# Kernel optimization log

Hardware: AMD Instinct MI355X
Metric: run time of the kernel (lower is better)

The kernel has to match this reference:

```python
import jax, jax.numpy as jnp
import numpy as np

W_DIM, T_DIM = 300, 100
IN = W_DIM + T_DIM        # 400, also LSTM hidden size
H = IN                    # hiddenSize
BI = 2 * H                # 800, biLSTM output per step
MLP_IN = 2 * BI           # 1600
VOCAB, NTAGS = 50000, 50
SEQ = 320


def _lstm_dir(xs, w_ih, w_hh, b_ih, b_hh, h0, c0, reverse):
    # xs: [T, d_in]; PyTorch gate order i, f, g, o
    if reverse:
        xs = xs[::-1]
    def step(carry, x):
        h, c = carry
        g = x @ w_ih.T + h @ w_hh.T + b_ih + b_hh
        i, f, gc, o = jnp.split(g, 4)
        i, f, o = jax.nn.sigmoid(i), jax.nn.sigmoid(f), jax.nn.sigmoid(o)
        c = f * c + i * jnp.tanh(gc)
        h = o * jnp.tanh(c)
        return (h, c), h
    _, ys = jax.lax.scan(step, (h0, c0), xs)
    return ys[::-1] if reverse else ys


def _bilstm(x, params, h0, c0):
    # x: [T, IN]; h0/c0: [4, H] ordered (l0 fwd, l0 bwd, l1 fwd, l1 bwd)
    out = x
    for layer in range(2):
        p_f = params[layer][0]
        p_b = params[layer][1]
        yf = _lstm_dir(out, *p_f, h0[2 * layer],     c0[2 * layer],     False)
        yb = _lstm_dir(out, *p_b, h0[2 * layer + 1], c0[2 * layer + 1], True)
        out = jnp.concatenate([yf, yb], axis=-1)  # [T, 2H]
    return out


def setup_inputs() -> dict:
    key = jax.random.key(0)
    ks = iter(jax.random.split(key, 32))
    inp = {}
    inp['words'] = jax.random.randint(next(ks), (SEQ,), 0, VOCAB)
    inp['tags'] = jax.random.randint(next(ks), (SEQ,), 0, NTAGS)
    inp['arcs'] = jax.random.randint(next(ks), (SEQ + 1,), 0, SEQ + 1)
    inp['word_emb'] = jax.random.normal(next(ks), (VOCAB, W_DIM), jnp.float32) * 0.1
    inp['tag_emb'] = jax.random.normal(next(ks), (NTAGS, T_DIM), jnp.float32) * 0.1
    inp['h0'] = jax.random.normal(next(ks), (4, H), jnp.float32)
    inp['c0'] = jax.random.normal(next(ks), (4, H), jnp.float32)
    s = 1.0 / np.sqrt(H)
    for layer, d_in in ((0, IN), (1, BI)):
        for suf in ('', 'r'):
            inp[f'w_ih_l{layer}{suf}'] = jax.random.uniform(next(ks), (4 * H, d_in), jnp.float32, -s, s)
            inp[f'w_hh_l{layer}{suf}'] = jax.random.uniform(next(ks), (4 * H, H), jnp.float32, -s, s)
            inp[f'b_ih_l{layer}{suf}'] = jax.random.uniform(next(ks), (4 * H,), jnp.float32, -s, s)
            inp[f'b_hh_l{layer}{suf}'] = jax.random.uniform(next(ks), (4 * H,), jnp.float32, -s, s)
    inp['mlp_w1'] = jax.random.normal(next(ks), (MLP_IN, MLP_IN), jnp.float32) * 0.02
    inp['mlp_b1'] = jnp.zeros((MLP_IN,), jnp.float32)
    inp['mlp_w2'] = jax.random.normal(next(ks), (1, MLP_IN), jnp.float32) * 0.02
    inp['mlp_b2'] = jnp.zeros((1,), jnp.float32)
    return inp


def reference(words, tags, arcs, word_emb, tag_emb, h0, c0,
              w_ih_l0, w_hh_l0, b_ih_l0, b_hh_l0,
              w_ih_l0r, w_hh_l0r, b_ih_l0r, b_hh_l0r,
              w_ih_l1, w_hh_l1, b_ih_l1, b_hh_l1,
              w_ih_l1r, w_hh_l1r, b_ih_l1r, b_hh_l1r,
              mlp_w1, mlp_b1, mlp_w2, mlp_b2):
    n = words.shape[0]
    x = jnp.concatenate([word_emb[words], tag_emb[tags]], axis=1)  # [n, IN]
    params = (((w_ih_l0, w_hh_l0, b_ih_l0, b_hh_l0), (w_ih_l0r, w_hh_l0r, b_ih_l0r, b_hh_l0r)),
              ((w_ih_l1, w_hh_l1, b_ih_l1, b_hh_l1), (w_ih_l1r, w_hh_l1r, b_ih_l1r, b_hh_l1r)))
    hv = _bilstm(x, params, h0, c0)  # [n, BI]
    # pairwise MLP: concat(h_head, h_dep) @ W1.T == h_head @ W1a.T + h_dep @ W1b.T
    w1a, w1b = mlp_w1[:, :BI], mlp_w1[:, BI:]
    a = hv @ w1a.T  # [n, MLP_IN], head part
    b = hv @ w1b.T  # [n, MLP_IN], dep part
    hid = jax.nn.relu(a[:, None, :] + b[None, :, :] + mlp_b1)  # [n, n, MLP_IN]
    scores = jnp.einsum('ndk,ok->nd', hid, mlp_w2)[..., 0] if mlp_w2.shape[0] != 1 else (hid @ mlp_w2[0] + mlp_b2[0])  # [n, n]
    offdiag = 1.0 - jnp.eye(n, dtype=scores.dtype)
    score_tensor = jnp.zeros((n + 1, n + 1), scores.dtype)
    score_tensor = score_tensor.at[0, 0].set(1.0)
    score_tensor = score_tensor.at[1:, 1:].set(scores * offdiag)
    return score_tensor
```

## Files before the change

kernel.cpp:

```cpp
#include <hip/hip_runtime.h>
#include <hip/hip_bf16.h>
#include <hip/hip_fp16.h>

#define SEQ   320
#define GATES 1600
#define NCOL  3200
#define GDW   16
#define RPW   25

typedef _Float16 half2v __attribute__((ext_vector_type(2)));
typedef _Float16 f16x8  __attribute__((ext_vector_type(8)));
typedef float    f32x4  __attribute__((ext_vector_type(4)));
union H2U { unsigned u; half2v h; __half2 hh; };

__global__ __launch_bounds__(256) void prep_kernel(
    const int* __restrict__ words, const int* __restrict__ tags,
    const float* __restrict__ wemb, const float* __restrict__ temb,
    _Float16* __restrict__ Ah0,
    const float* __restrict__ bihl0,  const float* __restrict__ bhhl0,
    const float* __restrict__ bihl0r, const float* __restrict__ bhhl0r,
    const float* __restrict__ bihl1,  const float* __restrict__ bhhl1,
    const float* __restrict__ bihl1r, const float* __restrict__ bhhl1r,
    const float* __restrict__ mlpb1,
    float* __restrict__ bL0, float* __restrict__ bL1, float* __restrict__ bAB,
    const float* __restrict__ wih0, const float* __restrict__ wih0r,
    _Float16* __restrict__ BhA)
{
    const int b = blockIdx.x, t = threadIdx.x;
    if (b < 520) {
        int i = b * 256 + t;
        if (i >= SEQ * 416) return;
        int tt = i / 416, c = i % 416;
        float v = 0.f;
        if (c < 300)      v = wemb[(size_t)words[tt] * 300 + c];
        else if (c < 400) v = temb[(size_t)tags[tt] * 100 + (c - 300)];
        Ah0[i] = (_Float16)v;
    } else if (b < 533) {
        int g = (b - 520) * 256 + t;
        if (g >= NCOL) return;
        if (g < GATES) {
            bL0[g] = bihl0[g] + bhhl0[g];
            bL1[g] = bihl1[g] + bhhl1[g];
            bAB[g] = mlpb1[g];
        } else {
            int q = g - GATES;
            bL0[g] = bihl0r[q] + bhhl0r[q];
            bL1[g] = bihl1r[q] + bhhl1r[q];
            bAB[g] = 0.f;
        }
    } else {
        int i = (b - 533) * 256 + t;
        if (i >= NCOL * 416) return;
        int n = i / 416, k = i % 416;
        float v = 0.f;
        if (k < 400)
            v = (n < GATES) ? wih0[(size_t)n * 400 + k]
                            : wih0r[(size_t)(n - GATES) * 400 + k];
        BhA[i] = (_Float16)v;
    }
}

__global__ __launch_bounds__(256) void cvt2_kernel(
    const float* __restrict__ wih1, const float* __restrict__ wih1r,
    _Float16* __restrict__ BhB,
    const float* __restrict__ mlpw1, _Float16* __restrict__ BhA)
{
    const int b = blockIdx.x, t = threadIdx.x;
    if (b < 10000) {
        int i = b * 256 + t;
        if (i >= NCOL * 800) return;
        int n = i / 800, k = i % 800;
        BhB[i] = (_Float16)((n < GATES) ? wih1[(size_t)n * 800 + k]
                                        : wih1r[(size_t)(n - GATES) * 800 + k]);
    } else {
        int i = (b - 10000) * 256 + t;
        if (i >= NCOL * 800) return;
        int n = i / 800, k = i % 800;
        BhA[i] = (_Float16)((n < GATES) ? mlpw1[(size_t)n * 1600 + k]
                                        : mlpw1[(size_t)(n - GATES) * 1600 + 800 + k]);
    }
}

__global__ __launch_bounds__(256) void gemm_f16(
    const _Float16* __restrict__ A, int Kp,
    const _Float16* __restrict__ B,
    const float* __restrict__ bias, float* __restrict__ C)
{
    const int tid  = threadIdx.x;
    const int w    = tid >> 6, lane = tid & 63;
    const int quad = lane >> 4, l16 = lane & 15;
    const int mb   = blockIdx.y * 32 + (w & 1) * 16;
    const int n0   = blockIdx.x * 64 + (w >> 1) * 32;
    const _Float16* Arow = A + (size_t)(mb + l16) * Kp + quad * 8;
    const _Float16* B0r  = B + (size_t)(n0 + l16) * Kp + quad * 8;
    const _Float16* B1r  = B0r + (size_t)16 * Kp;
    f32x4 acc0 = {0.f, 0.f, 0.f, 0.f}, acc1 = {0.f, 0.f, 0.f, 0.f};
#pragma unroll 4
    for (int k0 = 0; k0 < Kp; k0 += 32) {
        f16x8 a  = *(const f16x8*)(Arow + k0);
        f16x8 b0 = *(const f16x8*)(B0r + k0);
        f16x8 b1 = *(const f16x8*)(B1r + k0);
        acc0 = __builtin_amdgcn_mfma_f32_16x16x32_f16(a, b0, acc0, 0, 0, 0);
        acc1 = __builtin_amdgcn_mfma_f32_16x16x32_f16(a, b1, acc1, 0, 0, 0);
    }
    const int mr = mb + quad * 4;
    float bn0 = bias[n0 + l16], bn1 = bias[n0 + 16 + l16];
#pragma unroll
    for (int r = 0; r < 4; ++r) {
        C[(size_t)(mr + r) * NCOL + n0 + l16]      = acc0[r] + bn0;
        C[(size_t)(mr + r) * NCOL + n0 + 16 + l16] = acc1[r] + bn1;
    }
}

__global__ __launch_bounds__(1024, 4) void lstm_layer(
    const float* __restrict__ gates,
    const float* __restrict__ whh_f, const float* __restrict__ whh_b,
    const float* __restrict__ h0f, const float* __restrict__ h0b,
    const float* __restrict__ c0f, const float* __restrict__ c0b,
    unsigned* __restrict__ ex,
    _Float16* __restrict__ ah)
{
    __shared__ unsigned h_pk[200];
    __shared__ float part[16][28];
    unsigned short* hs = (unsigned short*)h_pk;
    const int tid = threadIdx.x;
    const int dir = blockIdx.x >> 4;
    const int wg  = blockIdx.x & 15;
    const int j0  = wg * RPW;
    const float* whh = dir ? whh_b : whh_f;
    const float* h0d = dir ? h0b : h0f;
    const float* c0d = dir ? c0b : c0f;

    const int w    = tid >> 6;
    const int lane = tid & 63;
    const int g    = w & 3;
    const int kq   = w >> 2;
    const int half = lane & 1;
    const int r    = lane >> 1;
    const int jrow = j0 + (r < RPW ? r : RPW - 1);

    unsigned wr[26];
    {
        const float2* wp = (const float2*)(whh + (size_t)(g * 400 + jrow) * 400 +
                                           kq * 100 + 48 * half);
#pragma unroll
        for (int i = 0; i < 26; ++i) {
            H2U cv; float2 f = wp[i];
            cv.hh = __floats2half2_rn(f.x, f.y);
            wr[i] = (half == 0 && i >= 24) ? 0u : cv.u;
        }
    }

    const int pp = tid / 13;
    const int pd = tid - pp * 13;
    float c_prev = (tid < RPW) ? c0d[j0 + tid] : 0.f;

    for (int s = 0; s < 320; ++s) {
        const int row = dir ? (319 - s) : s;

        float gv0 = 0.f, gv1 = 0.f, gv2 = 0.f, gv3 = 0.f;
        if (tid < RPW) {
            const float* gx = gates + (size_t)row * NCOL + dir * GATES + j0 + tid;
            gv0 = gx[0]; gv1 = gx[400]; gv2 = gx[800]; gv3 = gx[1200];
        }

        if (s == 0) {
            if (tid < 100) {
                float4 f = ((const float4*)h0d)[tid];
                H2U a, b;
                a.hh = __floats2half2_rn(f.x, f.y);
                b.hh = __floats2half2_rn(f.z, f.w);
                ((uint2*)h_pk)[tid] = make_uint2(a.u, b.u);
            }
        } else if (tid < 208 && pp != wg) {
            const int rp = dir ? (row + 1) : (row - 1);
            const unsigned* src = ex + (((size_t)dir * GDW + pp) * SEQ + rp) * 16 + pd;
            unsigned v;
            for (;;) {
                v = __hip_atomic_load(src, __ATOMIC_RELAXED, __HIP_MEMORY_SCOPE_AGENT);
                if ((v & 0xFFFFu) != 0xFFFFu &&
                    (pd == 12 || (v >> 16) != 0xFFFFu)) break;
            }
            const int hb = pp * RPW + pd * 2;
            hs[hb] = (unsigned short)(v & 0xFFFFu);
            if (pd < 12) hs[hb + 1] = (unsigned short)(v >> 16);
        }
        __syncthreads();

        {
            const uint2* hp2 = (const uint2*)h_pk + kq * 25 + 12 * half;
            float acc = 0.f;
#pragma unroll
            for (int i = 0; i < 13; ++i) {
                uint2 hv2 = hp2[i];
                H2U w0, w1, x0, x1;
                w0.u = wr[2 * i]; w1.u = wr[2 * i + 1];
                x0.u = hv2.x;     x1.u = hv2.y;
                acc = __builtin_amdgcn_fdot2(w0.h, x0.h, acc, false);
                acc = __builtin_amdgcn_fdot2(w1.h, x1.h, acc, false);
            }
            acc += __shfl_xor(acc, 1, 64);
            if (half == 0 && r < RPW) part[w][r] = acc;
        }
        __syncthreads();

        float hv = 0.f;
        if (tid < RPW) {
            float gi = gv0 + ((part[0][tid] + part[4][tid]) + (part[8][tid]  + part[12][tid]));
            float gf = gv1 + ((part[1][tid] + part[5][tid]) + (part[9][tid]  + part[13][tid]));
            float gg = gv2 + ((part[2][tid] + part[6][tid]) + (part[10][tid] + part[14][tid]));
            float go = gv3 + ((part[3][tid] + part[7][tid]) + (part[11][tid] + part[15][tid]));
            float iv = 1.f / (1.f + __expf(-gi));
            float fv = 1.f / (1.f + __expf(-gf));
            float ov = 1.f / (1.f + __expf(-go));
            float tg = 1.f - 2.f / (1.f + __expf(2.f * gg));
            c_prev = fv * c_prev + iv * tg;
            float tc = 1.f - 2.f / (1.f + __expf(2.f * c_prev));
            hv = ov * tc;
        }
        if (w == 0) {
            int i0 = 2 * lane     < 63 ? 2 * lane     : 63;
            int i1 = 2 * lane + 1 < 63 ? 2 * lane + 1 : 63;
            float xlo = __shfl(hv, i0, 64);
            float xhi = __shfl(hv, i1, 64);
            if (lane < 13) {
                H2U pk;
                pk.hh = __floats2half2_rn(xlo, (2 * lane + 1 < RPW) ? xhi : 0.f);
                __hip_atomic_store(ex + (((size_t)dir * GDW + wg) * SEQ + row) * 16 + lane,
                                   pk.u, __ATOMIC_RELAXED, __HIP_MEMORY_SCOPE_AGENT);
            }
            if (tid < RPW) {
                ah[(size_t)row * 800 + dir * 400 + j0 + tid] = (_Float16)hv;
                H2U o; o.hh = __floats2half2_rn(hv, 0.f);
                hs[RPW * wg + tid] = (unsigned short)(o.u & 0xFFFFu);
            }
        }
    }
}

__global__ __launch_bounds__(256) void scores_kernel(
    const float* __restrict__ ab, const float* __restrict__ w2,
    const float* __restrict__ b2, float* __restrict__ out)
{
    if (blockIdx.y == 20) {
        int i = blockIdx.x * 256 + threadIdx.y * 16 + threadIdx.x;
        if (blockIdx.x < 2 && i < 321) {
            out[i]               = (i == 0) ? 1.f : 0.f;
            out[(size_t)i * 321] = (i == 0) ? 1.f : 0.f;
        }
        return;
    }
    __shared__ float a_s[16 * 132];
    __shared__ float b_s[16 * 132];
    __shared__ float w_s[128];
    const int tx = threadIdx.x, ty = threadIdx.y;
    const int tid = ty * 16 + tx;
    const int n0 = blockIdx.y * 16, d0 = blockIdx.x * 16;
    float acc = 0.f;
    for (int kc = 0; kc < 1600; kc += 128) {
        for (int i = tid; i < 16 * 128; i += 256) {
            int r = i >> 7, c = i & 127;
            a_s[r * 132 + c] = ab[(size_t)(n0 + r) * NCOL + kc + c];
            b_s[r * 132 + c] = ab[(size_t)(d0 + r) * NCOL + 1600 + kc + c];
        }
        if (tid < 128) w_s[tid] = w2[kc + tid];
        __syncthreads();
#pragma unroll
        for (int k = 0; k < 128; k += 4) {
            float4 av = *(const float4*)&a_s[ty * 132 + k];
            float4 bv = *(const float4*)&b_s[tx * 132 + k];
            float4 wv = *(const float4*)&w_s[k];
            acc += fmaxf(av.x + bv.x, 0.f) * wv.x;
            acc += fmaxf(av.y + bv.y, 0.f) * wv.y;
            acc += fmaxf(av.z + bv.z, 0.f) * wv.z;
            acc += fmaxf(av.w + bv.w, 0.f) * wv.w;
        }
        __syncthreads();
    }
    int n = n0 + ty, d = d0 + tx;
    out[(size_t)(n + 1) * 321 + (d + 1)] = (n == d) ? 0.f : (acc + b2[0]);
}

extern "C" void kernel_launch(void* const* d_in, const int* in_sizes, int n_in,
                              void* d_out, int out_size, void* d_ws, size_t ws_size,
                              hipStream_t stream)
{
    const int*   words    = (const int*)d_in[0];
    const int*   tags     = (const int*)d_in[1];
    const float* wemb     = (const float*)d_in[3];
    const float* temb     = (const float*)d_in[4];
    const float* h0       = (const float*)d_in[5];
    const float* c0       = (const float*)d_in[6];
    const float* w_ih_l0  = (const float*)d_in[7];
    const float* w_hh_l0  = (const float*)d_in[8];
    const float* b_ih_l0  = (const float*)d_in[9];
    const float* b_hh_l0  = (const float*)d_in[10];
    const float* w_ih_l0r = (const float*)d_in[11];
    const float* w_hh_l0r = (const float*)d_in[12];
    const float* b_ih_l0r = (const float*)d_in[13];
    const float* b_hh_l0r = (const float*)d_in[14];
    const float* w_ih_l1  = (const float*)d_in[15];
    const float* w_hh_l1  = (const float*)d_in[16];
    const float* b_ih_l1  = (const float*)d_in[17];
    const float* b_hh_l1  = (const float*)d_in[18];
    const float* w_ih_l1r = (const float*)d_in[19];
    const float* w_hh_l1r = (const float*)d_in[20];
    const float* b_ih_l1r = (const float*)d_in[21];
    const float* b_hh_l1r = (const float*)d_in[22];
    const float* mlp_w1   = (const float*)d_in[23];
    const float* mlp_b1   = (const float*)d_in[24];
    const float* mlp_w2   = (const float*)d_in[25];
    const float* mlp_b2   = (const float*)d_in[26];
    float* out = (float*)d_out;

    float* ws      = (float*)d_ws;
    float*    gates  = ws;
    float*    biasL0 = ws + 1024000;
    float*    biasL1 = ws + 1027200;
    float*    biasAB = ws + 1030400;
    unsigned* ex     = (unsigned*)(ws + 1033600);
    _Float16* Ah0    = (_Float16*)(ws + 1361280);
    _Float16* Ah1    = (_Float16*)(ws + 1427840);
    _Float16* Ah2    = (_Float16*)(ws + 1555840);
    _Float16* BhA    = (_Float16*)(ws + 1683840);
    _Float16* BhB    = (_Float16*)(ws + 2963840);
    unsigned* ex0 = ex, *ex1 = ex + 163840;

    hipMemsetAsync(ex, 0xFF, 327680u * 4, stream);

    prep_kernel<<<5733, 256, 0, stream>>>(
        words, tags, wemb, temb, Ah0,
        b_ih_l0, b_hh_l0, b_ih_l0r, b_hh_l0r,
        b_ih_l1, b_hh_l1, b_ih_l1r, b_hh_l1r,
        mlp_b1, biasL0, biasL1, biasAB, w_ih_l0, w_ih_l0r, BhA);

    gemm_f16<<<dim3(50, 10), 256, 0, stream>>>(Ah0, 416, BhA, biasL0, gates);
    cvt2_kernel<<<20000, 256, 0, stream>>>(w_ih_l1, w_ih_l1r, BhB, mlp_w1, BhA);
    lstm_layer<<<2 * GDW, 1024, 0, stream>>>(gates, w_hh_l0, w_hh_l0r,
                                             h0, h0 + 400, c0, c0 + 400, ex0, Ah1);
    gemm_f16<<<dim3(50, 10), 256, 0, stream>>>(Ah1, 800, BhB, biasL1, gates);
    lstm_layer<<<2 * GDW, 1024, 0, stream>>>(gates, w_hh_l1, w_hh_l1r,
                                             h0 + 800, h0 + 1200, c0 + 800, c0 + 1200,
                                             ex1, Ah2);
    gemm_f16<<<dim3(50, 10), 256, 0, stream>>>(Ah2, 800, BhA, biasAB, gates);

    scores_kernel<<<dim3(20, 21), dim3(16, 16), 0, stream>>>(gates, mlp_w2, mlp_b2, out);
}
```

Before: 1.353 ms.

## Restructure LSTM recurrence into 25 small blocks per direction with double-buffered h

Re-partitions the persistent LSTM recurrence from 16 blocks of 1024 threads (25 rows each) into 25 blocks of 256 threads per direction, each owning 16 hidden units. Each thread now keeps two weight rows in registers and reduces gate partials with wave shuffles, so the per-step shared-memory partial buffer and one barrier go away. The hidden-state exchange becomes one packed word per row pair with a simpler full-word poll, and a double-buffered h in shared memory replaces the single buffer. The exchange buffer is shared across layers and re-memset between them, which adds cross-block polling traffic because there are more producer blocks.

```diff
diff --git a/kernel.cpp b/kernel.cpp
--- a/kernel.cpp
+++ b/kernel.cpp
@@ -5,8 +5,8 @@
 #define SEQ   320
 #define GATES 1600
 #define NCOL  3200
-#define GDW   16
-#define RPW   25
+#define GDW   25
+#define RPW   16
 
 typedef _Float16 half2v __attribute__((ext_vector_type(2)));
 typedef _Float16 f16x8  __attribute__((ext_vector_type(8)));
@@ -112,7 +112,7 @@
     }
 }
 
-__global__ __launch_bounds__(1024, 4) void lstm_layer(
+__global__ __launch_bounds__(256) void lstm_layer(
     const float* __restrict__ gates,
     const float* __restrict__ whh_f, const float* __restrict__ whh_b,
     const float* __restrict__ h0f, const float* __restrict__ h0b,
@@ -120,120 +120,126 @@
     unsigned* __restrict__ ex,
     _Float16* __restrict__ ah)
 {
-    __shared__ unsigned h_pk[200];
-    __shared__ float part[16][28];
-    unsigned short* hs = (unsigned short*)h_pk;
+    __shared__ __align__(16) unsigned hbuf[2][224];
     const int tid = threadIdx.x;
-    const int dir = blockIdx.x >> 4;
-    const int wg  = blockIdx.x & 15;
-    const int j0  = wg * RPW;
+    const int dir = blockIdx.x >= GDW;
+    const int wg  = blockIdx.x - dir * GDW;
     const float* whh = dir ? whh_b : whh_f;
     const float* h0d = dir ? h0b : h0f;
     const float* c0d = dir ? c0b : c0f;
 
-    const int w    = tid >> 6;
-    const int lane = tid & 63;
-    const int g    = w & 3;
-    const int kq   = w >> 2;
-    const int half = lane & 1;
-    const int r    = lane >> 1;
-    const int jrow = j0 + (r < RPW ? r : RPW - 1);
-
-    unsigned wr[26];
+    const int rp = tid >> 5;
+    const int g  = (tid >> 3) & 3;
+    const int ks = tid & 7;
+    const int jA = wg * RPW + 2 * rp;
+
+    unsigned wrA[25], wrB[25];
     {
-        const float2* wp = (const float2*)(whh + (size_t)(g * 400 + jrow) * 400 +
-                                           kq * 100 + 48 * half);
+        const float2* wA = (const float2*)(whh + ((size_t)g * 400 + jA) * 400 + 50 * ks);
+        const float2* wB = (const float2*)(whh + ((size_t)g * 400 + jA + 1) * 400 + 50 * ks);
 #pragma unroll
-        for (int i = 0; i < 26; ++i) {
-            H2U cv; float2 f = wp[i];
-            cv.hh = __floats2half2_rn(f.x, f.y);
-            wr[i] = (half == 0 && i >= 24) ? 0u : cv.u;
-        }
-    }
-
-    const int pp = tid / 13;
-    const int pd = tid - pp * 13;
-    float c_prev = (tid < RPW) ? c0d[j0 + tid] : 0.f;
-
-    for (int s = 0; s < 320; ++s) {
-        const int row = dir ? (319 - s) : s;
-
-        float gv0 = 0.f, gv1 = 0.f, gv2 = 0.f, gv3 = 0.f;
-        if (tid < RPW) {
-            const float* gx = gates + (size_t)row * NCOL + dir * GATES + j0 + tid;
-            gv0 = gx[0]; gv1 = gx[400]; gv2 = gx[800]; gv3 = gx[1200];
-        }
+        for (int i = 0; i < 25; ++i) {
+            float2 fa = wA[i], fb = wB[i];
+            H2U ca, cbu;
+            ca.hh  = __floats2half2_rn(fa.x, fa.y);
+            cbu.hh = __floats2half2_rn(fb.x, fb.y);
+            wrA[i] = ca.u; wrB[i] = cbu.u;
+        }
+    }
+
+    int bp = 0, pollq = 0;
+    if (tid < 192) {
+        bp = tid >> 3; bp += (bp >= wg);
+        int q = bp * 8 + (tid & 7);
+        pollq = (q / 25) * 28 + q % 25;
+    }
+    const int qown    = wg * 8 + rp;
+    const int ownaddr = (qown / 25) * 28 + qown % 25;
+    const float* gbase = gates + dir * GATES + g * 400 + jA;
+    unsigned* exq = ex + ((size_t)(dir * GDW + wg) * SEQ) * 16 + rp;
+    unsigned* ahq = (unsigned*)ah + dir * 200 + wg * 8 + rp;
+
+    float cA = c0d[jA], cB = c0d[jA + 1];
+
+    for (int s = 0; s < SEQ; ++s) {
+        const int row = dir ? (SEQ - 1 - s) : s;
+        const int cb  = s & 1;
+        float2 gv = *(const float2*)(gbase + (size_t)row * NCOL);
 
         if (s == 0) {
-            if (tid < 100) {
-                float4 f = ((const float4*)h0d)[tid];
-                H2U a, b;
-                a.hh = __floats2half2_rn(f.x, f.y);
-                b.hh = __floats2half2_rn(f.z, f.w);
-                ((uint2*)h_pk)[tid] = make_uint2(a.u, b.u);
+            if (tid < 200) {
+                float2 f = ((const float2*)h0d)[tid];
+                H2U a; a.hh = __floats2half2_rn(f.x, f.y);
+                hbuf[0][(tid / 25) * 28 + tid % 25] = a.u;
             }
-        } else if (tid < 208 && pp != wg) {
-            const int rp = dir ? (row + 1) : (row - 1);
-            const unsigned* src = ex + (((size_t)dir * GDW + pp) * SEQ + rp) * 16 + pd;
+        } else if (tid < 192) {
+            const int rprev = dir ? row + 1 : row - 1;
+            const unsigned* src = ex + (((size_t)dir * GDW + bp) * SEQ + rprev) * 16 + (tid & 7);
             unsigned v;
-            for (;;) {
+            do {
                 v = __hip_atomic_load(src, __ATOMIC_RELAXED, __HIP_MEMORY_SCOPE_AGENT);
-                if ((v & 0xFFFFu) != 0xFFFFu &&
-                    (pd == 12 || (v >> 16) != 0xFFFFu)) break;
-            }
-            const int hb = pp * RPW + pd * 2;
-            hs[hb] = (unsigned short)(v & 0xFFFFu);
-            if (pd < 12) hs[hb + 1] = (unsigned short)(v >> 16);
+            } while (v == 0xFFFFFFFFu);
+            hbuf[cb][pollq] = v;
         }
         __syncthreads();
 
+        const unsigned* hb = &hbuf[cb][ks * 28];
+        float accA = 0.f, accB = 0.f;
+#pragma unroll
+        for (int i = 0; i < 6; ++i) {
+            uint4 hq = *(const uint4*)(hb + 4 * i);
+            H2U x0, x1, x2, x3, wa, wb;
+            x0.u = hq.x; x1.u = hq.y; x2.u = hq.z; x3.u = hq.w;
+            wa.u = wrA[4*i+0]; wb.u = wrB[4*i+0];
+            accA = __builtin_amdgcn_fdot2(wa.h, x0.h, accA, false);
+            accB = __builtin_amdgcn_fdot2(wb.h, x0.h, accB, false);
+            wa.u = wrA[4*i+1]; wb.u = wrB[4*i+1];
+            accA = __builtin_amdgcn_fdot2(wa.h, x1.h, accA, false);
+            accB = __builtin_amdgcn_fdot2(wb.h, x1.h, accB, false);
+            wa.u = wrA[4*i+2]; wb.u = wrB[4*i+2];
+            accA = __builtin_amdgcn_fdot2(wa.h, x2.h, accA, false);
+            accB = __builtin_amdgcn_fdot2(wb.h, x2.h, accB, false);
+            wa.u = wrA[4*i+3]; wb.u = wrB[4*i+3];
+            accA = __builtin_amdgcn_fdot2(wa.h, x3.h, accA, false);
+            accB = __builtin_amdgcn_fdot2(wb.h, x3.h, accB, false);
+        }
         {
-            const uint2* hp2 = (const uint2*)h_pk + kq * 25 + 12 * half;
-            float acc = 0.f;
-#pragma unroll
-            for (int i = 0; i < 13; ++i) {
-                uint2 hv2 = hp2[i];
-                H2U w0, w1, x0, x1;
-                w0.u = wr[2 * i]; w1.u = wr[2 * i + 1];
-                x0.u = hv2.x;     x1.u = hv2.y;
-                acc = __builtin_amdgcn_fdot2(w0.h, x0.h, acc, false);
-                acc = __builtin_amdgcn_fdot2(w1.h, x1.h, acc, false);
-            }
-            acc += __shfl_xor(acc, 1, 64);
-            if (half == 0 && r < RPW) part[w][r] = acc;
-        }
-        __syncthreads();
-
-        float hv = 0.f;
-        if (tid < RPW) {
-            float gi = gv0 + ((part[0][tid] + part[4][tid]) + (part[8][tid]  + part[12][tid]));
-            float gf = gv1 + ((part[1][tid] + part[5][tid]) + (part[9][tid]  + part[13][tid]));
-            float gg = gv2 + ((part[2][tid] + part[6][tid]) + (part[10][tid] + part[14][tid]));
-            float go = gv3 + ((part[3][tid] + part[7][tid]) + (part[11][tid] + part[15][tid]));
-            float iv = 1.f / (1.f + __expf(-gi));
-            float fv = 1.f / (1.f + __expf(-gf));
-            float ov = 1.f / (1.f + __expf(-go));
-            float tg = 1.f - 2.f / (1.f + __expf(2.f * gg));
-            c_prev = fv * c_prev + iv * tg;
-            float tc = 1.f - 2.f / (1.f + __expf(2.f * c_prev));
-            hv = ov * tc;
-        }
-        if (w == 0) {
-            int i0 = 2 * lane     < 63 ? 2 * lane     : 63;
-            int i1 = 2 * lane + 1 < 63 ? 2 * lane + 1 : 63;
-            float xlo = __shfl(hv, i0, 64);
-            float xhi = __shfl(hv, i1, 64);
-            if (lane < 13) {
-                H2U pk;
-                pk.hh = __floats2half2_rn(xlo, (2 * lane + 1 < RPW) ? xhi : 0.f);
-                __hip_atomic_store(ex + (((size_t)dir * GDW + wg) * SEQ + row) * 16 + lane,
-                                   pk.u, __ATOMIC_RELAXED, __HIP_MEMORY_SCOPE_AGENT);
-            }
-            if (tid < RPW) {
-                ah[(size_t)row * 800 + dir * 400 + j0 + tid] = (_Float16)hv;
-                H2U o; o.hh = __floats2half2_rn(hv, 0.f);
-                hs[RPW * wg + tid] = (unsigned short)(o.u & 0xFFFFu);
-            }
+            H2U xl, wa, wb; xl.u = hb[24];
+            wa.u = wrA[24]; wb.u = wrB[24];
+            accA = __builtin_amdgcn_fdot2(wa.h, xl.h, accA, false);
+            accB = __builtin_amdgcn_fdot2(wb.h, xl.h, accB, false);
+        }
+
+        accA += __shfl_xor(accA, 1); accA += __shfl_xor(accA, 2); accA += __shfl_xor(accA, 4);
+        accB += __shfl_xor(accB, 1); accB += __shfl_xor(accB, 2); accB += __shfl_xor(accB, 4);
+        accA += gv.x; accB += gv.y;
+
+        float a1 = __shfl_xor(accA, 8), a2 = __shfl_xor(accA, 16), a3 = __shfl_xor(accA, 24);
+        float b1 = __shfl_xor(accB, 8), b2 = __shfl_xor(accB, 16), b3 = __shfl_xor(accB, 24);
+        float giA = g==0?accA : g==1?a1 : g==2?a2 : a3;
+        float gfA = g==1?accA : g==0?a1 : g==3?a2 : a3;
+        float ggA = g==2?accA : g==3?a1 : g==0?a2 : a3;
+        float goA = g==3?accA : g==2?a1 : g==1?a2 : a3;
+        float giB = g==0?accB : g==1?b1 : g==2?b2 : b3;
+        float gfB = g==1?accB : g==0?b1 : g==3?b2 : b3;
+        float ggB = g==2?accB : g==3?b1 : g==0?b2 : b3;
+        float goB = g==3?accB : g==2?b1 : g==1?b2 : b3;
+
+        float ivA = 1.f / (1.f + __expf(-giA)), fvA = 1.f / (1.f + __expf(-gfA));
+        float ovA = 1.f / (1.f + __expf(-goA)), tgA = 1.f - 2.f / (1.f + __expf(2.f * ggA));
+        float ivB = 1.f / (1.f + __expf(-giB)), fvB = 1.f / (1.f + __expf(-gfB));
+        float ovB = 1.f / (1.f + __expf(-goB)), tgB = 1.f - 2.f / (1.f + __expf(2.f * ggB));
+        cA = fvA * cA + ivA * tgA;
+        cB = fvB * cB + ivB * tgB;
+        float hA = ovA * (1.f - 2.f / (1.f + __expf(2.f * cA)));
+        float hB = ovB * (1.f - 2.f / (1.f + __expf(2.f * cB)));
+
+        if ((tid & 31) == 0) {
+            H2U pk; pk.hh = __floats2half2_rn(hA, hB);
+            __hip_atomic_store(exq + (size_t)row * 16, pk.u,
+                               __ATOMIC_RELAXED, __HIP_MEMORY_SCOPE_AGENT);
+            ahq[(size_t)row * 400] = pk.u;
+            hbuf[cb ^ 1][ownaddr] = pk.u;
         }
     }
 }
@@ -319,14 +325,13 @@
     float*    biasL1 = ws + 1027200;
     float*    biasAB = ws + 1030400;
     unsigned* ex     = (unsigned*)(ws + 1033600);
-    _Float16* Ah0    = (_Float16*)(ws + 1361280);
-    _Float16* Ah1    = (_Float16*)(ws + 1427840);
-    _Float16* Ah2    = (_Float16*)(ws + 1555840);
-    _Float16* BhA    = (_Float16*)(ws + 1683840);
-    _Float16* BhB    = (_Float16*)(ws + 2963840);
-    unsigned* ex0 = ex, *ex1 = ex + 163840;
-
-    hipMemsetAsync(ex, 0xFF, 327680u * 4, stream);
+    _Float16* Ah0    = (_Float16*)(ws + 1289600);
+    _Float16* Ah1    = (_Float16*)(ws + 1356160);
+    _Float16* Ah2    = (_Float16*)(ws + 1484160);
+    _Float16* BhA    = (_Float16*)(ws + 1612160);
+    _Float16* BhB    = (_Float16*)(ws + 2892160);
+
+    hipMemsetAsync(ex, 0xFF, 256000u * 4, stream);
 
     prep_kernel<<<5733, 256, 0, stream>>>(
         words, tags, wemb, temb, Ah0,
@@ -336,12 +341,13 @@
 
     gemm_f16<<<dim3(50, 10), 256, 0, stream>>>(Ah0, 416, BhA, biasL0, gates);
     cvt2_kernel<<<20000, 256, 0, stream>>>(w_ih_l1, w_ih_l1r, BhB, mlp_w1, BhA);
-    lstm_layer<<<2 * GDW, 1024, 0, stream>>>(gates, w_hh_l0, w_hh_l0r,
-                                             h0, h0 + 400, c0, c0 + 400, ex0, Ah1);
+    lstm_layer<<<2 * GDW, 256, 0, stream>>>(gates, w_hh_l0, w_hh_l0r,
+                                            h0, h0 + 400, c0, c0 + 400, ex, Ah1);
+    hipMemsetAsync(ex, 0xFF, 256000u * 4, stream);
     gemm_f16<<<dim3(50, 10), 256, 0, stream>>>(Ah1, 800, BhB, biasL1, gates);
-    lstm_layer<<<2 * GDW, 1024, 0, stream>>>(gates, w_hh_l1, w_hh_l1r,
-                                             h0 + 800, h0 + 1200, c0 + 800, c0 + 1200,
-                                             ex1, Ah2);
+    lstm_layer<<<2 * GDW, 256, 0, stream>>>(gates, w_hh_l1, w_hh_l1r,
+                                            h0 + 800, h0 + 1200, c0 + 800, c0 + 1200,
+                                            ex, Ah2);
     gemm_f16<<<dim3(50, 10), 256, 0, stream>>>(Ah2, 800, BhA, biasAB, gates);
 
     scores_kernel<<<dim3(20, 21), dim3(16, 16), 0, stream>>>(gates, mlp_w2, mlp_b2, out);
```

New measurement: 1.458 ms. 7.7% more time.
